# Performance work log

Measured on AMD Instinct MI355X. Metric: run time of the kernel, lower is better.

## Reference

```python
import jax, jax.numpy as jnp
import numpy as np
from jax import lax

V, DM, DS, DC, EXP = 32000, 1024, 16, 4, 2
DI = EXP * DM            # 2048 inner dim
DTR = (DM + 15) // 16    # 64  dt_rank
B, L = 2, 2048


def setup_inputs() -> dict:
    key = jax.random.key(0)
    ks = jax.random.split(key, 10)
    tokens = jax.random.randint(ks[0], (B, L), 0, V)
    embed = jax.random.normal(ks[1], (V, DM), jnp.float32) * 0.02
    in_proj_w = jax.random.normal(ks[2], (2 * DI, DM), jnp.float32) * (DM ** -0.5)
    conv_w = jax.random.normal(ks[3], (DI, DC), jnp.float32) * 0.2
    conv_b = jnp.zeros((DI,), jnp.float32)
    x_proj_w = jax.random.normal(ks[4], (DTR + 2 * DS, DI), jnp.float32) * (DI ** -0.5)
    dt_proj_w = jax.random.normal(ks[5], (DI, DTR), jnp.float32) * (DTR ** -0.5)
    # mamba-style dt bias init: softplus^{-1}(uniform in [1e-3, ~0.1])
    dt = 1e-3 + jax.random.uniform(ks[6], (DI,), jnp.float32) * 0.1
    dt_proj_b = jnp.log(jnp.expm1(dt))
    # S4D-real init: A = -[1..d_state] per channel
    A_log = jnp.log(jnp.broadcast_to(jnp.arange(1, DS + 1, dtype=jnp.float32), (DI, DS)))
    D = jnp.ones((DI,), jnp.float32)
    out_proj_w = jax.random.normal(ks[7], (DM, DI), jnp.float32) * (DI ** -0.5)
    head_w = jax.random.normal(ks[8], (V, DM), jnp.float32) * 0.02
    head_b = jnp.zeros((V,), jnp.float32)
    return dict(tokens=tokens, embed=embed, in_proj_w=in_proj_w, conv_w=conv_w,
                conv_b=conv_b, x_proj_w=x_proj_w, dt_proj_w=dt_proj_w,
                dt_proj_b=dt_proj_b, A_log=A_log, D=D, out_proj_w=out_proj_w,
                head_w=head_w, head_b=head_b)


def mamba_block(emb, in_proj_w, conv_w, conv_b, x_proj_w, dt_proj_w, dt_proj_b,
                A_log, D, out_proj_w):
    # emb: (B, L, DM)
    xz = jnp.einsum('bld,ed->ble', emb, in_proj_w)      # (B, L, 2*DI)
    x, z = jnp.split(xz, 2, axis=-1)
    # depthwise causal conv1d over time, then SiLU
    xt = x.transpose(0, 2, 1)                            # (B, DI, L)
    xc = lax.conv_general_dilated(xt, conv_w[:, None, :], (1,), [(DC - 1, 0)],
                                  feature_group_count=DI)
    x = jax.nn.silu(xc + conv_b[:, None]).transpose(0, 2, 1)  # (B, L, DI)
    # input-dependent dt, B, C
    dbc = jnp.einsum('bld,ed->ble', x, x_proj_w)         # (B, L, DTR+2*DS)
    dt = dbc[..., :DTR]
    Bm = dbc[..., DTR:DTR + DS]                          # (B, L, DS)
    Cm = dbc[..., DTR + DS:]                             # (B, L, DS)
    dt = jax.nn.softplus(jnp.einsum('blr,dr->bld', dt, dt_proj_w) + dt_proj_b)
    A = -jnp.exp(A_log)                                  # (DI, DS)

    def step(h, inp):
        dt_t, B_t, C_t, u_t = inp                        # (B,DI),(B,DS),(B,DS),(B,DI)
        dA = jnp.exp(dt_t[:, :, None] * A)               # (B, DI, DS)
        h = dA * h + dt_t[:, :, None] * B_t[:, None, :] * u_t[:, :, None]
        y = jnp.einsum('bds,bs->bd', h, C_t)
        return h, y

    h0 = jnp.zeros((x.shape[0], DI, DS), x.dtype)
    _, ys = lax.scan(step, h0, (dt.transpose(1, 0, 2), Bm.transpose(1, 0, 2),
                                Cm.transpose(1, 0, 2), x.transpose(1, 0, 2)))
    y = ys.transpose(1, 0, 2) + x * D                    # skip connection D*u
    y = y * jax.nn.silu(z)                               # gate
    return jnp.einsum('bld,ed->ble', y, out_proj_w)      # (B, L, DM)


def reference(tokens, embed, in_proj_w, conv_w, conv_b, x_proj_w, dt_proj_w,
              dt_proj_b, A_log, D, out_proj_w, head_w, head_b):
    emb = embed[tokens]                                  # (B, L, DM)
    y = mamba_block(emb, in_proj_w, conv_w, conv_b, x_proj_w, dt_proj_w,
                    dt_proj_b, A_log, D, out_proj_w)
    return jnp.einsum('bld,vd->blv', y, head_w) + head_b  # (B, L, V) logits
```

## Files before the change

### kernel.cpp

```cpp
#include <hip/hip_runtime.h>

typedef unsigned short ushort_t;
typedef __bf16 bf16x8 __attribute__((ext_vector_type(8)));
typedef float f32x4 __attribute__((ext_vector_type(4)));

constexpr int V_  = 32000;
constexpr int DM_ = 1024;
constexpr int DS_ = 16;
constexpr int DI_ = 2048;
constexpr int DTR_= 64;
constexpr int B_  = 2;
constexpr int L_  = 2048;
constexpr int M_  = B_ * L_;
constexpr int NXZ_= 2 * DI_;

constexpr size_t OFF_W_IN   = 0;
constexpr size_t OFF_W_OUT  = OFF_W_IN   + (size_t)NXZ_*DM_*2;
constexpr size_t OFF_W_HEAD = OFF_W_OUT  + (size_t)DM_*DI_*2;
constexpr size_t OFF_EMB    = OFF_W_HEAD + (size_t)V_*DM_*2;
constexpr size_t OFF_XZ     = OFF_EMB    + (size_t)M_*DM_*2;
constexpr size_t OFF_X      = OFF_XZ     + (size_t)M_*NXZ_*4;
constexpr size_t OFF_DBC    = OFF_X      + (size_t)M_*DI_*4;
constexpr size_t OFF_DT     = OFF_DBC    + (size_t)M_*96*4;
constexpr size_t OFF_Y      = OFF_DT     + (size_t)M_*DI_*4;
constexpr size_t OFF_MO     = OFF_Y      + (size_t)M_*DI_*2;

__device__ __forceinline__ ushort_t f2bf(float f) {
  union { float f; unsigned u; } v; v.f = f;
  unsigned r = v.u + 0x7FFFu + ((v.u >> 16) & 1u);
  return (ushort_t)(r >> 16);
}

__device__ __forceinline__ void async16(const void* g, void* l) {
  __builtin_amdgcn_global_load_lds(
      (const __attribute__((address_space(1))) unsigned int*)g,
      (__attribute__((address_space(3))) unsigned int*)l, 16, 0, 0);
}

__global__ __launch_bounds__(256) void cvt_bf16_kernel(
    const float* __restrict__ in, ushort_t* __restrict__ out, int n4) {
  int i = blockIdx.x * 256 + threadIdx.x;
  if (i >= n4) return;
  float4 v = ((const float4*)in)[i];
  ushort4 o;
  o.x = f2bf(v.x); o.y = f2bf(v.y); o.z = f2bf(v.z); o.w = f2bf(v.w);
  ((ushort4*)out)[i] = o;
}

__global__ __launch_bounds__(256) void gather_kernel(
    const int* __restrict__ tokens, const float* __restrict__ embed,
    ushort_t* __restrict__ out) {
  int i = blockIdx.x * 256 + threadIdx.x;
  int row = i >> 8;
  int c4 = i & 255;
  int tok = tokens[row];
  float4 v = ((const float4*)(embed + (size_t)tok * DM_))[c4];
  ushort4 o;
  o.x = f2bf(v.x); o.y = f2bf(v.y); o.z = f2bf(v.z); o.w = f2bf(v.w);
  ((ushort4*)out)[(size_t)row * 256 + c4] = o;
}

template <int EPI>
__global__ __launch_bounds__(256) void gemm_bt_kernel(
    const ushort_t* __restrict__ A, const ushort_t* __restrict__ Bw,
    float* __restrict__ Cf, ushort_t* __restrict__ Cb,
    const float* __restrict__ bias, int Ncols, int K) {
  __shared__ __attribute__((aligned(16))) ushort_t lds_a[4 * 128 * 8];
  __shared__ __attribute__((aligned(16))) ushort_t lds_b[4 * 128 * 8];
  const int tid  = threadIdx.x;
  const int lane = tid & 63;
  const int wave = tid >> 6;
  const int wm = wave & 1;
  const int wn = wave >> 1;

  const int q8  = gridDim.x >> 3;
  const int bid = blockIdx.x;
  const int swz = (bid & 7) * q8 + (bid >> 3);
  const int row0 = (swz & 31) << 7;
  const int col0 = (swz >> 5) << 7;

  f32x4 acc[4][4];
#pragma unroll
  for (int i = 0; i < 4; ++i)
#pragma unroll
    for (int j = 0; j < 4; ++j) acc[i][j] = f32x4{0.f, 0.f, 0.f, 0.f};

  const int sA0 = 2 * wave, sA1 = 2 * wave + 1;
  const int iA0 = sA0 * 64 + lane, iA1 = sA1 * 64 + lane;
  const ushort_t* pa0 = A  + (size_t)(row0 + (iA0 & 127)) * K + (iA0 >> 7) * 8;
  const ushort_t* pa1 = A  + (size_t)(row0 + (iA1 & 127)) * K + (iA1 >> 7) * 8;
  const ushort_t* pb0 = Bw + (size_t)(col0 + (iA0 & 127)) * K + (iA0 >> 7) * 8;
  const ushort_t* pb1 = Bw + (size_t)(col0 + (iA1 & 127)) * K + (iA1 >> 7) * 8;
  ushort_t* la0 = lds_a + sA0 * 512;
  ushort_t* la1 = lds_a + sA1 * 512;
  ushort_t* lb0 = lds_b + sA0 * 512;
  ushort_t* lb1 = lds_b + sA1 * 512;

  const int q = lane >> 4;
  const int r = lane & 15;

  for (int k0 = 0; k0 < K; k0 += 32) {
    async16(pa0 + k0, la0);
    async16(pa1 + k0, la1);
    async16(pb0 + k0, lb0);
    async16(pb1 + k0, lb1);
    __syncthreads();
    bf16x8 af[4], bfr[4];
#pragma unroll
    for (int i = 0; i < 4; ++i) {
      af[i]  = *(const bf16x8*)(lds_a + ((size_t)q * 128 + wm * 64 + i * 16 + r) * 8);
      bfr[i] = *(const bf16x8*)(lds_b + ((size_t)q * 128 + wn * 64 + i * 16 + r) * 8);
    }
#pragma unroll
    for (int i = 0; i < 4; ++i)
#pragma unroll
      for (int j = 0; j < 4; ++j)
        acc[i][j] = __builtin_amdgcn_mfma_f32_16x16x32_bf16(af[i], bfr[j], acc[i][j], 0, 0, 0);
    __syncthreads();
  }

#pragma unroll
  for (int i = 0; i < 4; ++i) {
#pragma unroll
    for (int j = 0; j < 4; ++j) {
      const int col = col0 + wn * 64 + j * 16 + r;
#pragma unroll
      for (int t = 0; t < 4; ++t) {
        const int row = row0 + wm * 64 + i * 16 + q * 4 + t;
        const float v = acc[i][j][t];
        if (EPI == 0) {
          Cf[(size_t)row * Ncols + col] = v;
        } else if (EPI == 1) {
          Cb[(size_t)row * Ncols + col] = f2bf(v);
        } else {
          Cf[(size_t)row * Ncols + col] = v + bias[col];
        }
      }
    }
  }
}

__global__ __launch_bounds__(256) void conv_silu_kernel(
    const float* __restrict__ xz, const float* __restrict__ conv_w,
    const float* __restrict__ conv_b, float* __restrict__ x_f32) {
  int i = blockIdx.x * 256 + threadIdx.x;
  int d = i & (DI_ - 1);
  int l = (i >> 11) & (L_ - 1);
  int b = i >> 22;
  const float4 w = ((const float4*)conv_w)[d];
  size_t rb = ((size_t)(b * L_ + l)) * NXZ_ + d;
  float acc = conv_b[d] + w.w * xz[rb];
  if (l >= 1) acc += w.z * xz[rb - NXZ_];
  if (l >= 2) acc += w.y * xz[rb - 2 * (size_t)NXZ_];
  if (l >= 3) acc += w.x * xz[rb - 3 * (size_t)NXZ_];
  float s = acc / (1.f + __expf(-acc));
  x_f32[i] = s;
}

__global__ __launch_bounds__(256) void xproj_kernel(
    const float* __restrict__ x, const float* __restrict__ w,
    float* __restrict__ dbc) {
  __shared__ __attribute__((aligned(16))) float sx[DI_];
  int row = blockIdx.x;
  const float4* xr = (const float4*)(x + (size_t)row * DI_);
  for (int j = threadIdx.x; j < DI_ / 4; j += 256) ((float4*)sx)[j] = xr[j];
  __syncthreads();
  if (threadIdx.x < 96) {
    const float4* wr = (const float4*)(w + (size_t)threadIdx.x * DI_);
    float acc = 0.f;
    for (int k = 0; k < DI_ / 4; ++k) {
      float4 a = ((const float4*)sx)[k];
      float4 bb = wr[k];
      acc += a.x * bb.x + a.y * bb.y + a.z * bb.z + a.w * bb.w;
    }
    dbc[(size_t)row * 96 + threadIdx.x] = acc;
  }
}

__global__ __launch_bounds__(256) void dtproj_kernel(
    const float* __restrict__ dbc, const float* __restrict__ w,
    const float* __restrict__ bias, float* __restrict__ dt_full) {
  __shared__ __attribute__((aligned(16))) float sdt[DTR_];
  int row = blockIdx.x;
  if (threadIdx.x < 16)
    ((float4*)sdt)[threadIdx.x] = ((const float4*)(dbc + (size_t)row * 96))[threadIdx.x];
  __syncthreads();
#pragma unroll
  for (int jj = 0; jj < 8; ++jj) {
    int d = threadIdx.x + jj * 256;
    const float4* wr = (const float4*)(w + (size_t)d * DTR_);
    float acc = bias[d];
#pragma unroll
    for (int k = 0; k < DTR_ / 4; ++k) {
      float4 a = ((const float4*)sdt)[k];
      float4 bb = wr[k];
      acc += a.x * bb.x + a.y * bb.y + a.z * bb.z + a.w * bb.w;
    }
    float sp = (acc > 15.f) ? acc : log1pf(__expf(acc));
    dt_full[(size_t)row * DI_ + d] = sp;
  }
}

__global__ __launch_bounds__(256) void scan_kernel(
    const float* __restrict__ dt_full, const float* __restrict__ x_f32,
    const float* __restrict__ xz, const float* __restrict__ dbc,
    const float* __restrict__ A_log, const float* __restrict__ Dvec,
    ushort_t* __restrict__ y_bf) {
  const int b  = blockIdx.x >> 7;
  const int d0 = (blockIdx.x & 127) << 4;
  const int tid = threadIdx.x;
  const int ch = tid >> 4;
  const int s  = tid & 15;
  const int d  = d0 + ch;
  const float a  = -__expf(A_log[(size_t)d * DS_ + s]);
  const float Dd = Dvec[d];
  float h = 0.f;
  __shared__ float s_dt[2][64][16], s_u[2][64][16], s_z[2][64][16],
                   s_B[2][64][16], s_C[2][64][16];
  const size_t rowbase = (size_t)b * L_;

  int ll_[4], j_[4];
#pragma unroll
  for (int rr = 0; rr < 4; ++rr) {
    int i = tid + rr * 256;
    ll_[rr] = i >> 4;
    j_[rr] = i & 15;
  }

#pragma unroll
  for (int rr = 0; rr < 4; ++rr) {
    const size_t row = rowbase + ll_[rr];
    s_dt[0][ll_[rr]][j_[rr]] = dt_full[row * DI_ + d0 + j_[rr]];
    s_u [0][ll_[rr]][j_[rr]] = x_f32 [row * DI_ + d0 + j_[rr]];
    s_z [0][ll_[rr]][j_[rr]] = xz    [row * NXZ_ + DI_ + d0 + j_[rr]];
    s_B [0][ll_[rr]][j_[rr]] = dbc   [row * 96 + DTR_ + j_[rr]];
    s_C [0][ll_[rr]][j_[rr]] = dbc   [row * 96 + DTR_ + DS_ + j_[rr]];
  }
  __syncthreads();

  for (int chunk = 0; chunk < L_ / 64; ++chunk) {
    const int cur = chunk & 1;
    const bool more = (chunk + 1 < L_ / 64);
    float rdt[4], ru[4], rz[4], rB[4], rC[4];
    if (more) {
      const int l1 = (chunk + 1) * 64;
#pragma unroll
      for (int rr = 0; rr < 4; ++rr) {
        const size_t row = rowbase + l1 + ll_[rr];
        rdt[rr] = dt_full[row * DI_ + d0 + j_[rr]];
        ru [rr] = x_f32 [row * DI_ + d0 + j_[rr]];
        rz [rr] = xz    [row * NXZ_ + DI_ + d0 + j_[rr]];
        rB [rr] = dbc   [row * 96 + DTR_ + j_[rr]];
        rC [rr] = dbc   [row * 96 + DTR_ + DS_ + j_[rr]];
      }
    }
#pragma unroll 1
    for (int t0 = 0; t0 < 64; t0 += 16) {
      float dA[16], dB[16], p[16];
#pragma unroll
      for (int t = 0; t < 16; ++t) {
        const float dtv = s_dt[cur][t0 + t][ch];
        const float uv  = s_u [cur][t0 + t][ch];
        dA[t] = __expf(dtv * a);
        dB[t] = dtv * uv * s_B[cur][t0 + t][s];
      }
#pragma unroll
      for (int t = 0; t < 16; ++t) {
        h = dA[t] * h + dB[t];
        p[t] = h * s_C[cur][t0 + t][s];
      }
#pragma unroll
      for (int t = 0; t < 16; ++t) p[t] += __shfl_xor(p[t], 8, 16);
#pragma unroll
      for (int t = 0; t < 16; ++t) p[t] += __shfl_xor(p[t], 4, 16);
#pragma unroll
      for (int t = 0; t < 16; ++t) p[t] += __shfl_xor(p[t], 2, 16);
#pragma unroll
      for (int t = 0; t < 16; ++t) p[t] += __shfl_xor(p[t], 1, 16);
      if (s == 0) {
#pragma unroll
        for (int t = 0; t < 16; ++t) {
          const float uv = s_u[cur][t0 + t][ch];
          float y = p[t] + uv * Dd;
          const float zv = s_z[cur][t0 + t][ch];
          y *= zv / (1.f + __expf(-zv));
          y_bf[(rowbase + chunk * 64 + t0 + t) * DI_ + d] = f2bf(y);
        }
      }
    }
    if (more) {
      const int nb = cur ^ 1;
#pragma unroll
      for (int rr = 0; rr < 4; ++rr) {
        s_dt[nb][ll_[rr]][j_[rr]] = rdt[rr];
        s_u [nb][ll_[rr]][j_[rr]] = ru [rr];
        s_z [nb][ll_[rr]][j_[rr]] = rz [rr];
        s_B [nb][ll_[rr]][j_[rr]] = rB [rr];
        s_C [nb][ll_[rr]][j_[rr]] = rC [rr];
      }
    }
    __syncthreads();
  }
}

extern "C" void kernel_launch(void* const* d_in, const int* in_sizes, int n_in,
                              void* d_out, int out_size, void* d_ws, size_t ws_size,
                              hipStream_t stream) {
  const int*   tokens     = (const int*)d_in[0];
  const float* embed      = (const float*)d_in[1];
  const float* in_proj_w  = (const float*)d_in[2];
  const float* conv_w     = (const float*)d_in[3];
  const float* conv_b     = (const float*)d_in[4];
  const float* x_proj_w   = (const float*)d_in[5];
  const float* dt_proj_w  = (const float*)d_in[6];
  const float* dt_proj_b  = (const float*)d_in[7];
  const float* A_log      = (const float*)d_in[8];
  const float* Dvec       = (const float*)d_in[9];
  const float* out_proj_w = (const float*)d_in[10];
  const float* head_w     = (const float*)d_in[11];
  const float* head_b     = (const float*)d_in[12];
  float* out = (float*)d_out;

  char* ws = (char*)d_ws;
  ushort_t* w_in_bf   = (ushort_t*)(ws + OFF_W_IN);
  ushort_t* w_out_bf  = (ushort_t*)(ws + OFF_W_OUT);
  ushort_t* w_head_bf = (ushort_t*)(ws + OFF_W_HEAD);
  ushort_t* emb_bf    = (ushort_t*)(ws + OFF_EMB);
  float*    xz        = (float*)   (ws + OFF_XZ);
  float*    x_f32     = (float*)   (ws + OFF_X);
  float*    dbc       = (float*)   (ws + OFF_DBC);
  float*    dt_full   = (float*)   (ws + OFF_DT);
  ushort_t* y_bf      = (ushort_t*)(ws + OFF_Y);
  ushort_t* mo_bf     = (ushort_t*)(ws + OFF_MO);

  cvt_bf16_kernel<<<(NXZ_ * DM_ / 4) / 256, 256, 0, stream>>>(in_proj_w, w_in_bf, NXZ_ * DM_ / 4);
  cvt_bf16_kernel<<<(DM_ * DI_ / 4) / 256, 256, 0, stream>>>(out_proj_w, w_out_bf, DM_ * DI_ / 4);
  cvt_bf16_kernel<<<(V_ * DM_ / 4) / 256, 256, 0, stream>>>(head_w, w_head_bf, V_ * DM_ / 4);
  gather_kernel<<<(M_ * DM_ / 4) / 256, 256, 0, stream>>>(tokens, embed, emb_bf);
  gemm_bt_kernel<0><<<(NXZ_ / 128) * (M_ / 128), 256, 0, stream>>>(
      emb_bf, w_in_bf, xz, nullptr, nullptr, NXZ_, DM_);
  conv_silu_kernel<<<(M_ * DI_) / 256, 256, 0, stream>>>(xz, conv_w, conv_b, x_f32);
  xproj_kernel<<<M_, 256, 0, stream>>>(x_f32, x_proj_w, dbc);
  dtproj_kernel<<<M_, 256, 0, stream>>>(dbc, dt_proj_w, dt_proj_b, dt_full);
  scan_kernel<<<B_ * (DI_ / 16), 256, 0, stream>>>(dt_full, x_f32, xz, dbc, A_log, Dvec, y_bf);
  gemm_bt_kernel<1><<<(DM_ / 128) * (M_ / 128), 256, 0, stream>>>(
      y_bf, w_out_bf, nullptr, mo_bf, nullptr, DM_, DI_);
  gemm_bt_kernel<2><<<(V_ / 128) * (M_ / 128), 256, 0, stream>>>(
      mo_bf, w_head_bf, out, nullptr, head_b, V_, DM_);
}
```

Baseline: 2.327 ms.

## Triple-buffer LDS tiles in bf16 GEMM with async prefetch two stages ahead

Replaces the single-buffered LDS load/compute loop in the shared GEMM kernel with a three-stage ring buffer. Global-to-LDS async copies for tile t+2 are issued before computing tile t, with explicit vmcnt waits and raw s_barrier calls instead of __syncthreads. This aims to hide global memory latency behind MFMA work. In exchange it triples LDS use per block, which may lower occupancy, and it relies on the async16 helper's per-lane LDS addressing staying correct with the new lane*8 offsets.

```diff
diff --git a/kernel.cpp b/kernel.cpp
--- a/kernel.cpp
+++ b/kernel.cpp
@@ -65,8 +65,8 @@
     const ushort_t* __restrict__ A, const ushort_t* __restrict__ Bw,
     float* __restrict__ Cf, ushort_t* __restrict__ Cb,
     const float* __restrict__ bias, int Ncols, int K) {
-  __shared__ __attribute__((aligned(16))) ushort_t lds_a[4 * 128 * 8];
-  __shared__ __attribute__((aligned(16))) ushort_t lds_b[4 * 128 * 8];
+  __shared__ __attribute__((aligned(16))) ushort_t lds_a[3][4 * 128 * 8];
+  __shared__ __attribute__((aligned(16))) ushort_t lds_b[3][4 * 128 * 8];
   const int tid  = threadIdx.x;
   const int lane = tid & 63;
   const int wave = tid >> 6;
@@ -91,32 +91,47 @@
   const ushort_t* pa1 = A  + (size_t)(row0 + (iA1 & 127)) * K + (iA1 >> 7) * 8;
   const ushort_t* pb0 = Bw + (size_t)(col0 + (iA0 & 127)) * K + (iA0 >> 7) * 8;
   const ushort_t* pb1 = Bw + (size_t)(col0 + (iA1 & 127)) * K + (iA1 >> 7) * 8;
-  ushort_t* la0 = lds_a + sA0 * 512;
-  ushort_t* la1 = lds_a + sA1 * 512;
-  ushort_t* lb0 = lds_b + sA0 * 512;
-  ushort_t* lb1 = lds_b + sA1 * 512;
 
   const int q = lane >> 4;
   const int r = lane & 15;
 
-  for (int k0 = 0; k0 < K; k0 += 32) {
-    async16(pa0 + k0, la0);
-    async16(pa1 + k0, la1);
-    async16(pb0 + k0, lb0);
-    async16(pb1 + k0, lb1);
-    __syncthreads();
+  const int NT = K >> 5;
+
+  auto stage = [&](int t) {
+    const int kk = t << 5;
+    const int bf = t % 3;
+    async16(pa0 + kk, &lds_a[bf][sA0 * 512 + lane * 8]);
+    async16(pa1 + kk, &lds_a[bf][sA1 * 512 + lane * 8]);
+    async16(pb0 + kk, &lds_b[bf][sA0 * 512 + lane * 8]);
+    async16(pb1 + kk, &lds_b[bf][sA1 * 512 + lane * 8]);
+  };
+
+
+  stage(0);
+  stage(1);
+
+#pragma unroll 1
+  for (int t = 0; t < NT; ++t) {
+    if (t + 2 < NT) stage(t + 2);
+    if (t + 2 < NT)      asm volatile("s_waitcnt vmcnt(8)" ::: "memory");
+    else if (t + 1 < NT) asm volatile("s_waitcnt vmcnt(4)" ::: "memory");
+    else                 asm volatile("s_waitcnt vmcnt(0)" ::: "memory");
+    __builtin_amdgcn_sched_barrier(0);
+    __builtin_amdgcn_s_barrier();
+    const int cb = t % 3;
     bf16x8 af[4], bfr[4];
 #pragma unroll
     for (int i = 0; i < 4; ++i) {
-      af[i]  = *(const bf16x8*)(lds_a + ((size_t)q * 128 + wm * 64 + i * 16 + r) * 8);
-      bfr[i] = *(const bf16x8*)(lds_b + ((size_t)q * 128 + wn * 64 + i * 16 + r) * 8);
+      af[i]  = *(const bf16x8*)(&lds_a[cb][((size_t)q * 128 + wm * 64 + i * 16 + r) * 8]);
+      bfr[i] = *(const bf16x8*)(&lds_b[cb][((size_t)q * 128 + wn * 64 + i * 16 + r) * 8]);
     }
 #pragma unroll
     for (int i = 0; i < 4; ++i)
 #pragma unroll
       for (int j = 0; j < 4; ++j)
         acc[i][j] = __builtin_amdgcn_mfma_f32_16x16x32_bf16(af[i], bfr[j], acc[i][j], 0, 0, 0);
-    __syncthreads();
+    __builtin_amdgcn_sched_barrier(0);
+    __builtin_amdgcn_s_barrier();
   }
 
 #pragma unroll
```

Result: no change. 2.311 ms (-0.7%).
